# Kernel tuning notes

Hardware: AMD Instinct MI355X
Metric: run time of the kernel (lower is better)

Reference implementation:

```python
import jax, jax.numpy as jnp
import numpy as np

H, W = 480, 640          # sensor resolution (self.dim)
N = 16_777_216           # number of events


def setup_inputs() -> dict:
    key = jax.random.key(0)
    k1, k2, k3, k4 = jax.random.split(key, 4)
    x = jax.random.randint(k1, (N,), 0, W).astype(jnp.float32)
    y = jax.random.randint(k2, (N,), 0, H).astype(jnp.float32)
    t = jax.random.uniform(k3, (N,), minval=1e-3, maxval=1.0)
    p = jax.random.randint(k4, (N,), 0, 2).astype(jnp.float32) * 2.0 - 1.0  # {-1, +1}
    events = jnp.stack([x, y, t, p], axis=1)  # [N, 4]
    return {"events": events}


def reference(events):
    # events: [N, 4] columns (x, y, t, p)
    x, y, t, p = events.T
    t = t / t.max()          # computed in original (unused for indexing)
    p = (p + 1.0) / 2.0      # {-1,1} -> {0,1}
    idx = (x + W * y + W * H * p).astype(jnp.int32)  # [N] flat voxel index
    # scatter-add event counts, then binarize (vox_ec[vox_ec > 0] = 1)
    vox = jnp.zeros(2 * H * W, dtype=events.dtype).at[idx].add(jnp.ones_like(x))
    vox = jnp.where(vox > 0, jnp.ones_like(vox), vox)
    return vox.reshape(-1, 2, H, W)  # [1, 2, H, W]
```

## Files before the change

kernel.cpp:

```cpp
#include <hip/hip_runtime.h>
#include <hip/hip_bf16.h>

#define EW 640
#define EH 480
#define NVOX (2 * EH * EW)
#define NWORDS (NVOX / 32)
#define BLKA 1024
#define NBLK_A 512

typedef float vf4 __attribute__((ext_vector_type(4)));

__device__ __forceinline__ int ev_idx(vf4 e) {
    float p01 = (e.w + 1.0f) * 0.5f;
    return (int)(e.x + (float)EW * e.y + (float)(EW * EH) * p01);
}

__global__ void __launch_bounds__(BLKA, 8)
event_bitmap_kernel(const vf4* __restrict__ events,
                    unsigned int* __restrict__ gbm, int n) {
    __shared__ unsigned int bm[NWORDS];
    for (int w = threadIdx.x; w < NWORDS; w += BLKA) bm[w] = 0u;
    __syncthreads();

    const int nth = gridDim.x * BLKA;
    int i = blockIdx.x * BLKA + threadIdx.x;
    for (; i + 3 * nth < n; i += 4 * nth) {
        vf4 e0 = events[i];
        vf4 e1 = events[i + nth];
        vf4 e2 = events[i + 2 * nth];
        vf4 e3 = events[i + 3 * nth];
        int x0 = ev_idx(e0), x1 = ev_idx(e1), x2 = ev_idx(e2), x3 = ev_idx(e3);
        atomicOr(&bm[x0 >> 5], 1u << (x0 & 31));
        atomicOr(&bm[x1 >> 5], 1u << (x1 & 31));
        atomicOr(&bm[x2 >> 5], 1u << (x2 & 31));
        atomicOr(&bm[x3 >> 5], 1u << (x3 & 31));
    }
    for (; i < n; i += nth) {
        vf4 e = events[i];
        int x = ev_idx(e);
        atomicOr(&bm[x >> 5], 1u << (x & 31));
    }
    __syncthreads();

    for (int w = threadIdx.x; w < NWORDS; w += BLKA) {
        unsigned int v = bm[w];
        if (v) atomicOr(&gbm[w], v);
    }
}

__global__ void __launch_bounds__(256)
expand_kernel(const unsigned int* __restrict__ gbm, float* __restrict__ out) {
    int t = blockIdx.x * 256 + threadIdx.x;
    unsigned int wv = gbm[t >> 3];
    int sh = (t & 7) * 4;
    vf4 v;
    v.x = (wv >> (sh + 0)) & 1u ? 1.0f : 0.0f;
    v.y = (wv >> (sh + 1)) & 1u ? 1.0f : 0.0f;
    v.z = (wv >> (sh + 2)) & 1u ? 1.0f : 0.0f;
    v.w = (wv >> (sh + 3)) & 1u ? 1.0f : 0.0f;
    ((vf4*)out)[t] = v;
}

extern "C" void kernel_launch(void* const* d_in, const int* in_sizes, int n_in,
                              void* d_out, int out_size, void* d_ws, size_t ws_size,
                              hipStream_t stream) {
    const vf4* events = (const vf4*)d_in[0];
    float* out = (float*)d_out;
    int n = in_sizes[0] / 4;

    unsigned int* gbm = (unsigned int*)d_ws;

    hipMemsetAsync(gbm, 0, NWORDS * sizeof(unsigned int), stream);

    event_bitmap_kernel<<<NBLK_A, BLKA, 0, stream>>>(events, gbm, n);
    expand_kernel<<<NVOX / 4 / 256, 256, 0, stream>>>(gbm, out);
}
```

Baseline: 366.5 us.

## Stream events into LDS with async global_load_lds in a per-wave pipeline

Replaces the direct strided global loads with per-wave contiguous chunks fetched by asynchronous global-to-LDS loads. Each wave keeps four chunks in flight in a private staging ring and waits on vmcnt before reading a slot. The grid is halved to 256 blocks, with one block per CU given the larger LDS footprint. The aim is to hide global load latency behind the LDS atomicOr work. In exchange the kernel runs at lower occupancy, and the fixed vmcnt(3) wait may not cover the final chunks once no further loads are issued.

```diff
diff --git a/kernel.cpp b/kernel.cpp
--- a/kernel.cpp
+++ b/kernel.cpp
@@ -5,8 +5,11 @@
 #define EH 480
 #define NVOX (2 * EH * EW)
 #define NWORDS (NVOX / 32)
-#define BLKA 1024
-#define NBLK_A 512
+#define BLK 1024
+#define GRID 256
+#define WAVES 16
+#define CHUNK 64
+#define DEPTH 4
 
 typedef float vf4 __attribute__((ext_vector_type(4)));
 
@@ -15,34 +18,52 @@
     return (int)(e.x + (float)EW * e.y + (float)(EW * EH) * p01);
 }
 
-__global__ void __launch_bounds__(BLKA, 8)
-event_bitmap_kernel(const vf4* __restrict__ events,
-                    unsigned int* __restrict__ gbm, int n) {
+__device__ __forceinline__ void async_ev16(const vf4* g, vf4* l) {
+    __builtin_amdgcn_global_load_lds(
+        (__attribute__((address_space(1))) void*)g,
+        (__attribute__((address_space(3))) void*)l,
+        16, 0, 0);
+}
+
+__global__ void __launch_bounds__(BLK, 4)
+event_bitmap_dma(const vf4* __restrict__ events,
+                 unsigned int* __restrict__ gbm, int n) {
     __shared__ unsigned int bm[NWORDS];
-    for (int w = threadIdx.x; w < NWORDS; w += BLKA) bm[w] = 0u;
+    __shared__ vf4 stage[WAVES * DEPTH * CHUNK];
+
+    for (int w = threadIdx.x; w < NWORDS; w += BLK) bm[w] = 0u;
     __syncthreads();
 
-    const int nth = gridDim.x * BLKA;
-    int i = blockIdx.x * BLKA + threadIdx.x;
-    for (; i + 3 * nth < n; i += 4 * nth) {
-        vf4 e0 = events[i];
-        vf4 e1 = events[i + nth];
-        vf4 e2 = events[i + 2 * nth];
-        vf4 e3 = events[i + 3 * nth];
-        int x0 = ev_idx(e0), x1 = ev_idx(e1), x2 = ev_idx(e2), x3 = ev_idx(e3);
-        atomicOr(&bm[x0 >> 5], 1u << (x0 & 31));
-        atomicOr(&bm[x1 >> 5], 1u << (x1 & 31));
-        atomicOr(&bm[x2 >> 5], 1u << (x2 & 31));
-        atomicOr(&bm[x3 >> 5], 1u << (x3 & 31));
+    const int wave = threadIdx.x >> 6;
+    const int lane = threadIdx.x & 63;
+    const int gw = blockIdx.x * WAVES + wave;
+    const int per_wave = n / (GRID * WAVES);
+    const int nchunks = per_wave / CHUNK;
+    const vf4* base = events + (size_t)gw * per_wave + lane;
+    vf4* bufs = &stage[wave * DEPTH * CHUNK];
+
+    const int pro = nchunks < DEPTH ? nchunks : DEPTH;
+    for (int c = 0; c < pro; ++c)
+        async_ev16(base + c * CHUNK, &bufs[c * CHUNK]);
+
+    for (int c = 0; c < nchunks; ++c) {
+        asm volatile("s_waitcnt vmcnt(3)" ::: "memory");
+        vf4 e = bufs[(c & (DEPTH - 1)) * CHUNK + lane];
+        int x = ev_idx(e);
+        atomicOr(&bm[x >> 5], 1u << (x & 31));
+        if (c + DEPTH < nchunks)
+            async_ev16(base + (c + DEPTH) * CHUNK, &bufs[(c & (DEPTH - 1)) * CHUNK]);
     }
-    for (; i < n; i += nth) {
+
+    const int done = GRID * WAVES * per_wave;
+    for (int i = done + blockIdx.x * BLK + threadIdx.x; i < n; i += GRID * BLK) {
         vf4 e = events[i];
         int x = ev_idx(e);
         atomicOr(&bm[x >> 5], 1u << (x & 31));
     }
+
     __syncthreads();
-
-    for (int w = threadIdx.x; w < NWORDS; w += BLKA) {
+    for (int w = threadIdx.x; w < NWORDS; w += BLK) {
         unsigned int v = bm[w];
         if (v) atomicOr(&gbm[w], v);
     }
@@ -72,6 +93,6 @@
 
     hipMemsetAsync(gbm, 0, NWORDS * sizeof(unsigned int), stream);
 
-    event_bitmap_kernel<<<NBLK_A, BLKA, 0, stream>>>(events, gbm, n);
+    event_bitmap_dma<<<GRID, BLK, 0, stream>>>(events, gbm, n);
     expand_kernel<<<NVOX / 4 / 256, 256, 0, stream>>>(gbm, out);
 }
```

New measurement: 370.9 us. About the same (+1.2%).
